# Performance work log

Measured on AMD Instinct MI355X. Metric: run time of the kernel, lower is better.

The kernel has to match this reference:

```python
import jax, jax.numpy as jnp
import numpy as np

K = 16        # max_points
S = 3         # num_scales
D_MODEL = 256
KDIM = 16
TAU = 1e-4
B_BATCH = 512


def _boundaries(k):
    edges = [(i, j) for i in range(k) for j in range(i + 1, k)]
    tris = [(i, j, kk) for i in range(k) for j in range(i + 1, k) for kk in range(j + 1, k)]
    E, T = len(edges), len(tris)
    B1 = np.zeros((k, E), np.float32)
    for e, (i, j) in enumerate(edges):
        B1[i, e] = -1.0
        B1[j, e] = 1.0
    e2i = {e: idx for idx, e in enumerate(edges)}
    B2 = np.zeros((E, T), np.float32)
    for t, (i, j, kk) in enumerate(tris):
        B2[e2i[(j, kk)], t] = 1.0
        B2[e2i[(i, kk)], t] = -1.0
        B2[e2i[(i, j)], t] = 1.0
    e_i = np.array([e[0] for e in edges], np.int32)
    e_j = np.array([e[1] for e in edges], np.int32)
    t_ij = np.array([e2i[(a, b)] for (a, b, c) in tris], np.int32)
    t_jk = np.array([e2i[(b, c)] for (a, b, c) in tris], np.int32)
    t_ik = np.array([e2i[(a, c)] for (a, b, c) in tris], np.int32)
    return B1, B2, e_i, e_j, t_ij, t_jk, t_ik


def setup_inputs() -> dict:
    key = jax.random.key(0)
    ks = jax.random.split(key, 8)
    d = D_MODEL
    B1, B2, e_i, e_j, t_ij, t_jk, t_ik = _boundaries(K)

    def lin(kk, fin, fout):
        return jax.random.normal(kk, (fin, fout), jnp.float32) / np.sqrt(fin).astype(np.float32)

    return dict(
        x=jax.random.normal(ks[0], (B_BATCH, K, d), jnp.float32),
        mask=jnp.ones((B_BATCH, K), jnp.float32),
        B1=jnp.asarray(B1), B2=jnp.asarray(B2), abs_B1=jnp.asarray(np.abs(B1)),
        e_i=jnp.asarray(e_i), e_j=jnp.asarray(e_j),
        t_ij=jnp.asarray(t_ij), t_jk=jnp.asarray(t_jk), t_ik=jnp.asarray(t_ik),
        log_scales=jnp.linspace(-1.5, 1.5, S).astype(jnp.float32),
        Wg=lin(ks[1], d, KDIM), bg=jnp.zeros((KDIM,), jnp.float32),
        Wv0=lin(ks[2], d, d * S), bv0=jnp.zeros((d * S,), jnp.float32),
        We=lin(ks[3], d, d * S), be=jnp.zeros((d * S,), jnp.float32),
        Wout=lin(ks[4], 2 * S * d, d), bout=jnp.zeros((d,), jnp.float32),
        g1=jnp.ones((d,), jnp.float32), b1=jnp.zeros((d,), jnp.float32),
        g2=jnp.ones((d,), jnp.float32), b2=jnp.zeros((d,), jnp.float32),
        Wf1=lin(ks[5], d, 4 * d), bf1=jnp.zeros((4 * d,), jnp.float32),
        Wf2=lin(ks[6], 4 * d, d), bf2=jnp.zeros((d,), jnp.float32),
    )


def _layernorm(x, g, b):
    mu = jnp.mean(x, -1, keepdims=True)
    var = jnp.mean(jnp.square(x - mu), -1, keepdims=True)
    return (x - mu) * jax.lax.rsqrt(var + 1e-5) * g + b


def _forward(x, mask, B1, B2, abs_B1, e_i, e_j, t_ij, t_jk, t_ik,
             log_scales, Wg, bg, Wv0, bv0, We, be, Wout, bout,
             g1, b1, g2, b2, Wf1, bf1, Wf2, bf2):
    B, Kp, d = x.shape
    E = B1.shape[1]
    residual = x
    x_norm = _layernorm(x, g1, b1)
    P = x_norm @ Wg + bg                                   # (B,K,k_dim)
    mask2 = mask[:, :, None] * mask[:, None, :]            # (B,K,K)
    # cdist (safe sqrt: zero diag, no NaN grads)
    pn = jnp.sum(P * P, -1)
    d2 = jnp.maximum(pn[:, :, None] + pn[:, None, :] - 2.0 * jnp.einsum('bik,bjk->bij', P, P), 0.0)
    Dm = jnp.where(d2 > 0, jnp.sqrt(jnp.where(d2 > 0, d2, 1.0)), 0.0) * mask2
    sigma_sq = jnp.square(jnp.exp(log_scales))             # (S,)
    A = jnp.exp(-(Dm * Dm)[:, None] / (2.0 * sigma_sq[None, :, None, None] + 1e-8)) * mask2[:, None]  # (B,S,K,K)
    W1 = A[:, :, e_i, e_j]                                 # (B,S,E) edge gather
    W2 = W1[:, :, t_ij] * W1[:, :, t_jk] * W1[:, :, t_ik]  # (B,S,T) triangle weights
    V0 = (x_norm @ Wv0 + bv0).reshape(B, Kp, S, d).transpose(0, 2, 1, 3)         # (B,S,K,d)
    E_raw = jnp.einsum('ke,bkd->bed', abs_B1, x_norm)                            # (B,E,d)
    E_in = (E_raw @ We + be).reshape(B, E, S, d).transpose(0, 2, 1, 3)           # (B,S,E,d)
    # L0 = B1 diag(W1) B1^T + tau I
    L0 = jnp.einsum('ke,bse,me->bskm', B1, W1, B1) + TAU * jnp.eye(Kp, dtype=x.dtype)
    M0 = jnp.einsum('bskm,bsmd->bskd', L0, V0)
    # L1 = B1^T diag(mask) B1 + B2 diag(W2) B2^T + tau I
    term_down = jnp.einsum('ke,bk,kf->bef', B1, mask, B1)                        # (B,E,E)
    term_up = jnp.einsum('et,bst,ft->bsef', B2, W2, B2)                          # (B,S,E,E)
    L1 = term_down[:, None] + term_up + TAU * jnp.eye(E, dtype=x.dtype)
    M1 = jnp.einsum('bsef,bsfd->bsed', L1, E_in)
    M1n = jnp.einsum('ke,bsed->bskd', abs_B1, M1)                                # edges -> nodes
    node_cat = M0.transpose(0, 2, 1, 3).reshape(B, Kp, S * d)
    edge_cat = M1n.transpose(0, 2, 1, 3).reshape(B, Kp, S * d)
    attn = jnp.concatenate([node_cat, edge_cat], -1) @ Wout + bout
    x2 = residual + attn                                   # dropout is identity in eval
    h = jax.nn.gelu(_layernorm(x2, g2, b2) @ Wf1 + bf1, approximate=False) @ Wf2 + bf2
    return x2 + h


def reference(x, mask, B1, B2, abs_B1, e_i, e_j, t_ij, t_jk, t_ik,
              log_scales, Wg, bg, Wv0, bv0, We, be, Wout, bout,
              g1, b1, g2, b2, Wf1, bf1, Wf2, bf2):
    return _forward(x, mask, B1, B2, abs_B1, e_i, e_j, t_ij, t_jk, t_ik,
                    log_scales, Wg, bg, Wv0, bv0, We, be, Wout, bout,
                    g1, b1, g2, b2, Wf1, bf1, Wf2, bf2)
```

## Files before the change

kernel.cpp:

```cpp
#include <hip/hip_runtime.h>
#include <math.h>

#define KN 16
#define DM 256
#define NS 3
#define NE 120
#define NT_TRI 560
#define NBATCH 512
#define TAUF 1e-4f
#define KAUG 1600

typedef unsigned short ushort_t;
typedef __attribute__((ext_vector_type(8))) short short8v;
typedef __attribute__((ext_vector_type(4))) short short4v;
typedef __attribute__((ext_vector_type(4))) float f32x4;

#define OFF_WSTACK 0u
#define OFF_WF1T   819200u
#define OFF_WF2T   1343488u
#define OFF_Z      1867776u
#define OFF_H      1867776u
#define OFF_LN2    28082176u

__device__ __forceinline__ ushort_t f2bf(float f) {
    union { float f; unsigned int u; } v; v.f = f;
    unsigned int r = v.u + 0x7FFFu + ((v.u >> 16) & 1u);
    return (ushort_t)(r >> 16);
}
__device__ __forceinline__ void gload_lds16(const void* g, void* l) {
    auto gp = (const __attribute__((address_space(1))) unsigned int*)(unsigned long long)(g);
    auto lp = (__attribute__((address_space(3))) unsigned int*)(unsigned long long)(l);
    __builtin_amdgcn_global_load_lds(gp, lp, 16, 0, 0);
}

__global__ __launch_bounds__(256) void prep_kernel(
    const float* __restrict__ Wv0, const float* __restrict__ bv0,
    const float* __restrict__ We,  const float* __restrict__ be,
    const float* __restrict__ Wout,
    const float* __restrict__ Wf1, const float* __restrict__ Wf2,
    ushort_t* __restrict__ wstack, ushort_t* __restrict__ wf1t,
    ushort_t* __restrict__ wf2t)
{
    __shared__ float lhs[16][DM];
    __shared__ float tile[64][65];
    const int bid = blockIdx.x;
    const int j = threadIdx.x;

    if (bid < 102) {
        const int m = bid / 17, by = bid % 17;
        const int path = m / 3, s = m % 3;
        const float* __restrict__ Wo = Wout + (size_t)m*DM*DM;
        if (by == 16) {
            const float* bv = (path == 0) ? bv0 : be;
            const float f = (path == 0) ? 1.0f : 0.5f;
            float acc = 0.f;
            for (int k = 0; k < DM; ++k)
                acc += bv[s*DM + k] * f * Wo[k*DM + j];
            wstack[(size_t)j*KAUG + 1536 + m] = f2bf(acc);
            if (m == 0)
                for (int c = 1542; c < KAUG; ++c)
                    wstack[(size_t)j*KAUG + c] = 0;
            return;
        }
        const float* src = (path == 0) ? Wv0 : We;
        const int i0 = by * 16;
        for (int r = 0; r < 16; ++r)
            lhs[r][j] = src[(size_t)(i0 + r)*(NS*DM) + s*DM + j];
        __syncthreads();
        float acc[16];
#pragma unroll
        for (int r = 0; r < 16; ++r) acc[r] = 0.f;
        for (int k = 0; k < DM; ++k) {
            const float w = Wo[k*DM + j];
#pragma unroll
            for (int r = 0; r < 16; ++r) acc[r] += lhs[r][k] * w;
        }
#pragma unroll
        for (int r = 0; r < 16; ++r)
            wstack[(size_t)j*KAUG + m*DM + i0 + r] = f2bf(acc[r]);
        return;
    }

    const float* in; ushort_t* outp; int R, C, rt, ct;
    if (bid < 166) {
        const int q = bid - 102;
        in = Wf1; outp = wf1t; R = 256; C = 1024;
        rt = (q >> 4) * 64; ct = (q & 15) * 64;
    } else {
        const int q = bid - 166;
        in = Wf2; outp = wf2t; R = 1024; C = 256;
        rt = (q >> 2) * 64; ct = (q & 3) * 64;
    }
#pragma unroll
    for (int q2 = 0; q2 < 16; ++q2) {
        const int idx = q2*256 + j;
        const int r = idx >> 6, c = idx & 63;
        tile[r][c] = in[(size_t)(rt + r)*C + ct + c];
    }
    __syncthreads();
#pragma unroll
    for (int q2 = 0; q2 < 16; ++q2) {
        const int idx = q2*256 + j;
        const int cc = idx >> 6, rr = idx & 63;
        outp[(size_t)(ct + cc)*R + rt + rr] = f2bf(tile[rr][cc]);
    }
}

__global__ __launch_bounds__(256) void attn_topo_kernel(
    const float* __restrict__ x, const float* __restrict__ mask,
    const int* __restrict__ e_i, const int* __restrict__ e_j,
    const int* __restrict__ t_ij, const int* __restrict__ t_jk, const int* __restrict__ t_ik,
    const float* __restrict__ log_scales,
    const float* __restrict__ Wg, const float* __restrict__ bg,
    const float* __restrict__ g1, const float* __restrict__ b1,
    ushort_t* __restrict__ Z)
{
    const int b = blockIdx.x;
    const int t = threadIdx.x;

    __shared__ float xnT[DM][KN+1];
    __shared__ float Plds[KN][KN];
    __shared__ float pn[KN];
    __shared__ float msk[KN];
    __shared__ float sA[NS][KN][KN];
    __shared__ int   eidx[KN][KN];
    __shared__ float Qm[KN][KN];
    __shared__ float P2m[KN][KN];
    __shared__ float HQ[KN][KN];
    __shared__ float Hup[NS][KN][KN];
    __shared__ float Tm[2*NS][KN][KN];

    {
        const int r = t >> 4, cg = (t & 15) * 16;
        const float* xr = x + (size_t)(b*KN + r)*DM + cg;
        float v[16]; float ssum = 0.f;
#pragma unroll
        for (int q = 0; q < 16; ++q) { v[q] = xr[q]; ssum += v[q]; }
#pragma unroll
        for (int o = 1; o < 16; o <<= 1) ssum += __shfl_xor(ssum, o);
        const float mu = ssum * (1.f/DM);
        float vsum = 0.f;
#pragma unroll
        for (int q = 0; q < 16; ++q) { float d = v[q]-mu; vsum += d*d; }
#pragma unroll
        for (int o = 1; o < 16; o <<= 1) vsum += __shfl_xor(vsum, o);
        const float rstd = rsqrtf(vsum*(1.f/DM) + 1e-5f);
#pragma unroll
        for (int q = 0; q < 16; ++q) {
            const int c = cg + q;
            xnT[c][r] = (v[q]-mu)*rstd*g1[c] + b1[c];
        }
        if (t < KN) msk[t] = mask[b*KN + t];
    }
    __syncthreads();

    {
        const int r = t & 15, c = t >> 4;
        float acc = bg[c];
        for (int k = 0; k < DM; ++k) acc += xnT[k][r] * Wg[k*KN + c];
        Plds[r][c] = acc;
    }
    __syncthreads();
    if (t < KN) {
        float s = 0.f;
#pragma unroll
        for (int k = 0; k < KN; ++k) { const float p = Plds[t][k]; s += p*p; }
        pn[t] = s;
    }
    __syncthreads();

    {
        const int r = t & 15, c = t >> 4;
        float dot = 0.f;
#pragma unroll
        for (int k = 0; k < KN; ++k) dot += Plds[r][k]*Plds[c][k];
        float d2 = pn[r] + pn[c] - 2.f*dot;
        const float m2 = msk[r]*msk[c];
        const float dm = (d2 > 0.f) ? sqrtf(d2)*m2 : 0.f;
        const float dmsq = dm*dm;
#pragma unroll
        for (int s = 0; s < NS; ++s) {
            const float sig2 = expf(2.f*log_scales[s]);
            sA[s][r][c] = expf(-dmsq/(2.f*sig2 + 1e-8f)) * m2;
        }
        eidx[r][c] = -1;
    }
    __syncthreads();
    if (t < NE) {
        const int i = e_i[t], jn = e_j[t];
        eidx[i][jn] = t; eidx[jn][i] = t;
    }
    __syncthreads();

    {
        const int n = t & 15, mcol = t >> 4;
        float q, p2;
        if (n != mcol) {
            const int e = eidx[n][mcol];
            if (e >= 0) { q = (mcol == e_j[e]) ? 1.f : -1.f; p2 = 1.f; }
            else        { q = 0.f; p2 = 0.f; }
        } else {
            q = 0.f; p2 = 0.f;
            for (int kk = 0; kk < KN; ++kk) {
                if (kk == n) continue;
                const int e = eidx[n][kk];
                if (e >= 0) { q += (n == e_j[e]) ? 1.f : -1.f; p2 += 1.f; }
            }
        }
        Qm[n][mcol] = q; P2m[n][mcol] = p2;
#pragma unroll
        for (int s = 0; s < NS; ++s) {
            float v;
            if (n != mcol) v = (eidx[n][mcol] >= 0) ? -sA[s][n][mcol] : 0.f;
            else {
                v = TAUF;
                for (int kk = 0; kk < KN; ++kk)
                    if (kk != n && eidx[n][kk] >= 0) v += sA[s][n][kk];
            }
            Tm[s][n][mcol] = v;
            Hup[s][n][mcol] = 0.f;
        }
    }
    __syncthreads();
    {
        const int n = t & 15, mcol = t >> 4;
        float acc = 0.f;
#pragma unroll
        for (int kk = 0; kk < KN; ++kk) acc += msk[kk]*Qm[n][kk]*Qm[mcol][kk];
        HQ[n][mcol] = acc;
    }
    for (int tt = t; tt < NT_TRI; tt += 256) {
        const int eij = t_ij[tt], ejk = t_jk[tt], eik = t_ik[tt];
        const int a0 = e_i[eij], a1 = e_j[eij];
        const int b0 = e_i[ejk], b1_ = e_j[ejk];
        const int c0 = e_i[eik], c1 = e_j[eik];
        float wprod[NS];
#pragma unroll
        for (int s = 0; s < NS; ++s)
            wprod[s] = sA[s][a0][a1] * sA[s][b0][b1_] * sA[s][c0][c1];
        int un[6]; int nu = 0;
        const int nodes[6] = {a0,a1,b0,b1_,c0,c1};
        for (int ii = 0; ii < 6; ++ii) {
            const int nd = nodes[ii]; bool seen = false;
            for (int jj = 0; jj < nu; ++jj) if (un[jj] == nd) seen = true;
            if (!seen) un[nu++] = nd;
        }
        float cf[6];
        for (int ii = 0; ii < nu; ++ii) {
            const int nd = un[ii];
            float c = 0.f;
            if (nd==b0 || nd==b1_) c += 1.f;
            if (nd==c0 || nd==c1 ) c -= 1.f;
            if (nd==a0 || nd==a1 ) c += 1.f;
            cf[ii] = c;
        }
        for (int ii = 0; ii < nu; ++ii) {
            if (cf[ii] == 0.f) continue;
            for (int jj = 0; jj < nu; ++jj) {
                if (cf[jj] == 0.f) continue;
                const float cc = cf[ii]*cf[jj];
#pragma unroll
                for (int s = 0; s < NS; ++s)
                    atomicAdd(&Hup[s][un[ii]][un[jj]], cc*wprod[s]);
            }
        }
    }
    __syncthreads();
    {
        const int n = t & 15, mcol = t >> 4;
#pragma unroll
        for (int s = 0; s < NS; ++s)
            Tm[NS+s][n][mcol] = HQ[n][mcol] + Hup[s][n][mcol] + TAUF*P2m[n][mcol];
    }
    __syncthreads();

    {
        const int j = t;
        float xr[KN];
#pragma unroll
        for (int mm = 0; mm < KN; ++mm) xr[mm] = xnT[j][mm];
        ushort_t* Zb = Z + (size_t)b*KN*KAUG;
        for (int m6 = 0; m6 < 6; ++m6) {
#pragma unroll
            for (int n = 0; n < KN; ++n) {
                float s = 0.f;
#pragma unroll
                for (int mm = 0; mm < KN; ++mm) s += Tm[m6][n][mm] * xr[mm];
                Zb[(size_t)n*KAUG + m6*DM + j] = f2bf(s);
            }
        }
        if (t < 96) {
            const int m6 = t >> 4, n = t & 15;
            float s = 0.f;
#pragma unroll
            for (int mm = 0; mm < KN; ++mm) s += Tm[m6][n][mm];
            Zb[(size_t)n*KAUG + 1536 + m6] = f2bf(s);
        }
        for (int idx = t; idx < 16*58; idx += 256) {
            const int n = idx / 58, c = 1542 + idx % 58;
            Zb[(size_t)n*KAUG + c] = 0;
        }
    }
}

template<int BM, int BN, int KD, int EPI>
__global__ __launch_bounds__(256) void gemm_lds(
    const ushort_t* __restrict__ A, const ushort_t* __restrict__ Bt,
    const float* __restrict__ bias, const float* __restrict__ resid,
    float* __restrict__ outF, ushort_t* __restrict__ outH, int ldo)
{
    constexpr int BK = 64;
    constexpr int MF = BM / 32, NF = BN / 32;
    __shared__ ushort_t lA[BM*BK];
    __shared__ ushort_t lB[BN*BK];
    const int t = threadIdx.x;
    const int w = t >> 6, l = t & 63;
    const int wm = w & 1, wn = w >> 1;
    const int lr = l & 15, lk = l >> 4;
    const int brow = blockIdx.x * BM;
    const int bcol = blockIdx.y * BN;

    f32x4 acc[MF][NF];
#pragma unroll
    for (int mf = 0; mf < MF; ++mf)
#pragma unroll
        for (int nt = 0; nt < NF; ++nt)
            acc[mf][nt] = (f32x4){0.f,0.f,0.f,0.f};

    const int byteoff = t * 16;

    for (int kc = 0; kc < KD/BK; ++kc) {
        if (kc) __syncthreads();
#pragma unroll
        for (int c = 0; c < BM/32; ++c) {
            const int bo = c*4096 + byteoff;
            const int row = bo >> 7, kb = bo & 127;
            gload_lds16(A + (size_t)(brow + row)*KD + kc*BK + (kb >> 1), lA + (bo >> 1));
        }
#pragma unroll
        for (int c = 0; c < BN/32; ++c) {
            const int bo = c*4096 + byteoff;
            const int row = bo >> 7, kb = bo & 127;
            gload_lds16(Bt + (size_t)(bcol + row)*KD + kc*BK + (kb >> 1), lB + (bo >> 1));
        }
        __syncthreads();
#pragma unroll
        for (int ks = 0; ks < 2; ++ks) {
            short8v af[MF], bfr[NF];
#pragma unroll
            for (int mf = 0; mf < MF; ++mf)
                af[mf] = *(const short8v*)(lA + (wm*(BM/2) + mf*16 + lr)*BK + ks*32 + lk*8);
#pragma unroll
            for (int nt = 0; nt < NF; ++nt)
                bfr[nt] = *(const short8v*)(lB + (wn*(BN/2) + nt*16 + lr)*BK + ks*32 + lk*8);
#pragma unroll
            for (int mf = 0; mf < MF; ++mf)
#pragma unroll
                for (int nt = 0; nt < NF; ++nt)
                    acc[mf][nt] = __builtin_amdgcn_mfma_f32_16x16x32_bf16(
                        af[mf], bfr[nt], acc[mf][nt], 0, 0, 0);
        }
    }

#pragma unroll
    for (int mf = 0; mf < MF; ++mf) {
#pragma unroll
        for (int nt = 0; nt < NF; ++nt) {
            const int col = bcol + wn*(BN/2) + nt*16 + lr;
#pragma unroll
            for (int rg = 0; rg < 4; ++rg) {
                const int row = brow + wm*(BM/2) + mf*16 + lk*4 + rg;
                const size_t o = (size_t)row * ldo + col;
                const float v = acc[mf][nt][rg];
                if (EPI == 1) {
                    const float u = v + bias[col];
                    const float a = 0.79788456080286536f*(u + 0.044715f*u*u*u);
                    outH[o] = f2bf(u / (1.f + __expf(-2.f*a)));
                } else if (EPI == 2) {
                    outF[o] = outF[o] + v + bias[col];
                } else {
                    outF[o] = resid[o] + v + bias[col];
                }
            }
        }
    }
}

__global__ __launch_bounds__(256) void ln_rows_kernel(
    const float* __restrict__ in, const float* __restrict__ g,
    const float* __restrict__ bvec, ushort_t* __restrict__ outv)
{
    const int row = blockIdx.x*4 + (threadIdx.x >> 6);
    const int l = threadIdx.x & 63;
    const float4 v = *(const float4*)(in + (size_t)row*DM + l*4);
    float s = v.x + v.y + v.z + v.w;
#pragma unroll
    for (int o = 1; o < 64; o <<= 1) s += __shfl_xor(s, o);
    const float mu = s * (1.f/DM);
    float d0 = v.x-mu, d1 = v.y-mu, d2 = v.z-mu, d3 = v.w-mu;
    float vs = d0*d0 + d1*d1 + d2*d2 + d3*d3;
#pragma unroll
    for (int o = 1; o < 64; o <<= 1) vs += __shfl_xor(vs, o);
    const float rstd = rsqrtf(vs*(1.f/DM) + 1e-5f);
    short4v o4;
    o4[0] = (short)f2bf(d0*rstd*g[l*4+0] + bvec[l*4+0]);
    o4[1] = (short)f2bf(d1*rstd*g[l*4+1] + bvec[l*4+1]);
    o4[2] = (short)f2bf(d2*rstd*g[l*4+2] + bvec[l*4+2]);
    o4[3] = (short)f2bf(d3*rstd*g[l*4+3] + bvec[l*4+3]);
    *(short4v*)(outv + (size_t)row*DM + l*4) = o4;
}

extern "C" void kernel_launch(void* const* d_in, const int* in_sizes, int n_in,
                              void* d_out, int out_size, void* d_ws, size_t ws_size,
                              hipStream_t stream) {
    const float* x          = (const float*)d_in[0];
    const float* mask       = (const float*)d_in[1];
    const int*   e_i        = (const int*)  d_in[5];
    const int*   e_j        = (const int*)  d_in[6];
    const int*   t_ij       = (const int*)  d_in[7];
    const int*   t_jk       = (const int*)  d_in[8];
    const int*   t_ik       = (const int*)  d_in[9];
    const float* log_scales = (const float*)d_in[10];
    const float* Wg         = (const float*)d_in[11];
    const float* bg         = (const float*)d_in[12];
    const float* Wv0        = (const float*)d_in[13];
    const float* bv0        = (const float*)d_in[14];
    const float* We         = (const float*)d_in[15];
    const float* be         = (const float*)d_in[16];
    const float* Wout       = (const float*)d_in[17];
    const float* bout       = (const float*)d_in[18];
    const float* g1         = (const float*)d_in[19];
    const float* b1         = (const float*)d_in[20];
    const float* g2         = (const float*)d_in[21];
    const float* b2         = (const float*)d_in[22];
    const float* Wf1        = (const float*)d_in[23];
    const float* bf1        = (const float*)d_in[24];
    const float* Wf2        = (const float*)d_in[25];
    const float* bf2        = (const float*)d_in[26];

    char* wsb = (char*)d_ws;
    ushort_t* wstack = (ushort_t*)(wsb + OFF_WSTACK);
    ushort_t* wf1t   = (ushort_t*)(wsb + OFF_WF1T);
    ushort_t* wf2t   = (ushort_t*)(wsb + OFF_WF2T);
    ushort_t* Z      = (ushort_t*)(wsb + OFF_Z);
    ushort_t* H      = (ushort_t*)(wsb + OFF_H);
    ushort_t* ln2    = (ushort_t*)(wsb + OFF_LN2);
    float*    out    = (float*)d_out;

    hipLaunchKernelGGL(prep_kernel, dim3(230), dim3(256), 0, stream,
                       Wv0, bv0, We, be, Wout, Wf1, Wf2, wstack, wf1t, wf2t);
    hipLaunchKernelGGL(attn_topo_kernel, dim3(NBATCH), dim3(256), 0, stream,
                       x, mask, e_i, e_j, t_ij, t_jk, t_ik, log_scales,
                       Wg, bg, g1, b1, Z);
    hipLaunchKernelGGL((gemm_lds<64,64,KAUG,3>), dim3(128,4), dim3(256), 0, stream,
                       Z, wstack, bout, x, out, (ushort_t*)nullptr, 256);
    hipLaunchKernelGGL(ln_rows_kernel, dim3(2048), dim3(256), 0, stream,
                       out, g2, b2, ln2);
    hipLaunchKernelGGL((gemm_lds<128,128,256,1>), dim3(64,8), dim3(256), 0, stream,
                       ln2, wf1t, bf1, (const float*)nullptr,
                       (float*)nullptr, H, 1024);
    hipLaunchKernelGGL((gemm_lds<64,64,1024,2>), dim3(128,4), dim3(256), 0, stream,
                       H, wf2t, bf2, (const float*)nullptr,
                       out, (ushort_t*)nullptr, 256);
}
```

Baseline: 127.7 us.

## Use MFMA for topology-matrix projection and register-parallel Wg projection in attn kernel

The per-block Z computation (6 small 16x16 matrices times a 16x256 normalized input) moves from scalar FMA loops to bf16 MFMA 16x16x32 instructions, with the normalized input kept in LDS as bf16 instead of transposed fp32. The Wg projection is now computed from register-resident normalized values with vector loads of Wg and a butterfly shuffle reduction, instead of each thread looping over 256 LDS values. Tm is padded to allow aligned vector reads. This cuts scalar ALU work and LDS traffic in the attention kernel, but adds bf16 rounding on the T matrices and on the normalized input before the product.

```diff
diff --git a/kernel.cpp b/kernel.cpp
--- a/kernel.cpp
+++ b/kernel.cpp
@@ -118,7 +118,7 @@
     const int b = blockIdx.x;
     const int t = threadIdx.x;
 
-    __shared__ float xnT[DM][KN+1];
+    __shared__ ushort_t xnb[KN][DM];
     __shared__ float Plds[KN][KN];
     __shared__ float pn[KN];
     __shared__ float msk[KN];
@@ -128,37 +128,82 @@
     __shared__ float P2m[KN][KN];
     __shared__ float HQ[KN][KN];
     __shared__ float Hup[NS][KN][KN];
-    __shared__ float Tm[2*NS][KN][KN];
-
-    {
-        const int r = t >> 4, cg = (t & 15) * 16;
+    __shared__ float Tm[2*NS][KN][20];
+
+    const int r  = t >> 4;
+    const int cg = (t & 15) * 16;
+
+    float xv[16];
+    {
         const float* xr = x + (size_t)(b*KN + r)*DM + cg;
-        float v[16]; float ssum = 0.f;
-#pragma unroll
-        for (int q = 0; q < 16; ++q) { v[q] = xr[q]; ssum += v[q]; }
+        float ssum = 0.f;
+#pragma unroll
+        for (int q = 0; q < 16; ++q) { xv[q] = xr[q]; ssum += xv[q]; }
 #pragma unroll
         for (int o = 1; o < 16; o <<= 1) ssum += __shfl_xor(ssum, o);
         const float mu = ssum * (1.f/DM);
         float vsum = 0.f;
 #pragma unroll
-        for (int q = 0; q < 16; ++q) { float d = v[q]-mu; vsum += d*d; }
+        for (int q = 0; q < 16; ++q) { float d = xv[q]-mu; vsum += d*d; }
 #pragma unroll
         for (int o = 1; o < 16; o <<= 1) vsum += __shfl_xor(vsum, o);
         const float rstd = rsqrtf(vsum*(1.f/DM) + 1e-5f);
+        short8v o0, o1;
 #pragma unroll
         for (int q = 0; q < 16; ++q) {
             const int c = cg + q;
-            xnT[c][r] = (v[q]-mu)*rstd*g1[c] + b1[c];
-        }
+            xv[q] = (xv[q]-mu)*rstd*g1[c] + b1[c];
+            if (q < 8) o0[q] = (short)f2bf(xv[q]); else o1[q-8] = (short)f2bf(xv[q]);
+        }
+        *(short8v*)&xnb[r][cg]     = o0;
+        *(short8v*)&xnb[r][cg+8]   = o1;
         if (t < KN) msk[t] = mask[b*KN + t];
     }
-    __syncthreads();
-
-    {
-        const int r = t & 15, c = t >> 4;
-        float acc = bg[c];
-        for (int k = 0; k < DM; ++k) acc += xnT[k][r] * Wg[k*KN + c];
-        Plds[r][c] = acc;
+
+    {
+        float part[16];
+#pragma unroll
+        for (int c = 0; c < 16; ++c) part[c] = 0.f;
+#pragma unroll
+        for (int q = 0; q < 16; ++q) {
+            const float xq = xv[q];
+            const float* wr = Wg + (size_t)(cg + q)*KN;
+            const f32x4 w0 = *(const f32x4*)(wr);
+            const f32x4 w1 = *(const f32x4*)(wr + 4);
+            const f32x4 w2 = *(const f32x4*)(wr + 8);
+            const f32x4 w3 = *(const f32x4*)(wr + 12);
+            part[0]  += xq*w0[0]; part[1]  += xq*w0[1]; part[2]  += xq*w0[2]; part[3]  += xq*w0[3];
+            part[4]  += xq*w1[0]; part[5]  += xq*w1[1]; part[6]  += xq*w1[2]; part[7]  += xq*w1[3];
+            part[8]  += xq*w2[0]; part[9]  += xq*w2[1]; part[10] += xq*w2[2]; part[11] += xq*w2[3];
+            part[12] += xq*w3[0]; part[13] += xq*w3[1]; part[14] += xq*w3[2]; part[15] += xq*w3[3];
+        }
+        const int b0 = t & 1, b1b = (t>>1)&1, b2 = (t>>2)&1, b3 = (t>>3)&1;
+        float p8[8];
+#pragma unroll
+        for (int c2 = 0; c2 < 8; ++c2) {
+            const float keep = b0 ? part[2*c2+1] : part[2*c2];
+            const float send = b0 ? part[2*c2]   : part[2*c2+1];
+            p8[c2] = keep + __shfl_xor(send, 1);
+        }
+        float p4[4];
+#pragma unroll
+        for (int c2 = 0; c2 < 4; ++c2) {
+            const float keep = b1b ? p8[2*c2+1] : p8[2*c2];
+            const float send = b1b ? p8[2*c2]   : p8[2*c2+1];
+            p4[c2] = keep + __shfl_xor(send, 2);
+        }
+        float p2v[2];
+#pragma unroll
+        for (int c2 = 0; c2 < 2; ++c2) {
+            const float keep = b2 ? p4[2*c2+1] : p4[2*c2];
+            const float send = b2 ? p4[2*c2]   : p4[2*c2+1];
+            p2v[c2] = keep + __shfl_xor(send, 4);
+        }
+        {
+            const float keep = b3 ? p2v[1] : p2v[0];
+            const float send = b3 ? p2v[0] : p2v[1];
+            Plds[r][t & 15] = keep + __shfl_xor(send, 8) + bg[t & 15];
+        }
     }
     __syncthreads();
     if (t < KN) {
@@ -170,20 +215,20 @@
     __syncthreads();
 
     {
-        const int r = t & 15, c = t >> 4;
+        const int rr = t & 15, c = t >> 4;
         float dot = 0.f;
 #pragma unroll
-        for (int k = 0; k < KN; ++k) dot += Plds[r][k]*Plds[c][k];
-        float d2 = pn[r] + pn[c] - 2.f*dot;
-        const float m2 = msk[r]*msk[c];
+        for (int k = 0; k < KN; ++k) dot += Plds[rr][k]*Plds[c][k];
+        float d2 = pn[rr] + pn[c] - 2.f*dot;
+        const float m2 = msk[rr]*msk[c];
         const float dm = (d2 > 0.f) ? sqrtf(d2)*m2 : 0.f;
         const float dmsq = dm*dm;
 #pragma unroll
         for (int s = 0; s < NS; ++s) {
             const float sig2 = expf(2.f*log_scales[s]);
-            sA[s][r][c] = expf(-dmsq/(2.f*sig2 + 1e-8f)) * m2;
-        }
-        eidx[r][c] = -1;
+            sA[s][rr][c] = expf(-dmsq/(2.f*sig2 + 1e-8f)) * m2;
+        }
+        eidx[rr][c] = -1;
     }
     __syncthreads();
     if (t < NE) {
@@ -275,20 +320,10 @@
     __syncthreads();
 
     {
-        const int j = t;
-        float xr[KN];
-#pragma unroll
-        for (int mm = 0; mm < KN; ++mm) xr[mm] = xnT[j][mm];
         ushort_t* Zb = Z + (size_t)b*KN*KAUG;
-        for (int m6 = 0; m6 < 6; ++m6) {
-#pragma unroll
-            for (int n = 0; n < KN; ++n) {
-                float s = 0.f;
-#pragma unroll
-                for (int mm = 0; mm < KN; ++mm) s += Tm[m6][n][mm] * xr[mm];
-                Zb[(size_t)n*KAUG + m6*DM + j] = f2bf(s);
-            }
-        }
+        const int w = t >> 6, l = t & 63;
+        const int lr = l & 15, lk = l >> 4;
+
         if (t < 96) {
             const int m6 = t >> 4, n = t & 15;
             float s = 0.f;
@@ -299,6 +334,38 @@
         for (int idx = t; idx < 16*58; idx += 256) {
             const int n = idx / 58, c = 1542 + idx % 58;
             Zb[(size_t)n*KAUG + c] = 0;
+        }
+
+        short8v bfr[4];
+#pragma unroll
+        for (int q4 = 0; q4 < 4; ++q4) {
+            const int jc = w*64 + q4*16 + lr;
+#pragma unroll
+            for (int i = 0; i < 8; ++i)
+                bfr[q4][i] = (lk < 2) ? (short)xnb[lk*8 + i][jc] : (short)0;
+        }
+#pragma unroll
+        for (int m6 = 0; m6 < 6; ++m6) {
+            short8v af = {0,0,0,0,0,0,0,0};
+            if (lk < 2) {
+                const f32x4 t0 = *(const f32x4*)&Tm[m6][lr][lk*8];
+                const f32x4 t1 = *(const f32x4*)&Tm[m6][lr][lk*8 + 4];
+                af[0] = (short)f2bf(t0[0]); af[1] = (short)f2bf(t0[1]);
+                af[2] = (short)f2bf(t0[2]); af[3] = (short)f2bf(t0[3]);
+                af[4] = (short)f2bf(t1[0]); af[5] = (short)f2bf(t1[1]);
+                af[6] = (short)f2bf(t1[2]); af[7] = (short)f2bf(t1[3]);
+            }
+#pragma unroll
+            for (int q4 = 0; q4 < 4; ++q4) {
+                f32x4 acc = {0.f,0.f,0.f,0.f};
+                acc = __builtin_amdgcn_mfma_f32_16x16x32_bf16(af, bfr[q4], acc, 0, 0, 0);
+                const int jc = w*64 + q4*16 + lr;
+#pragma unroll
+                for (int rg = 0; rg < 4; ++rg) {
+                    const int n = lk*4 + rg;
+                    Zb[(size_t)n*KAUG + m6*256 + jc] = f2bf(acc[rg]);
+                }
+            }
         }
     }
 }
```

Result: slower. 131.4 us (+2.9%).
